# Kernel optimization log

Hardware: AMD Instinct MI355X
Metric: run time of the kernel (lower is better)

## Reference

```python
import jax, jax.numpy as jnp
import numpy as np

B, C, L = 64, 50, 128      # tactic states, context entries per state, AST tokens per entry
V, S = 100008, 128          # vocab (sum of id tables), state/embed dim
OUT = 3


def _gru(h, x, w_ih, w_hh, b_ih, b_hh):
    # torch.nn.GRUCell math
    gi = x @ w_ih.T + b_ih            # [N, 3S]
    gh = h @ w_hh.T + b_hh
    i_r, i_z, i_n = jnp.split(gi, 3, axis=-1)
    h_r, h_z, h_n = jnp.split(gh, 3, axis=-1)
    r = jax.nn.sigmoid(i_r + h_r)
    z = jax.nn.sigmoid(i_z + h_z)
    n = jnp.tanh(i_n + r * h_n)
    return (1.0 - z) * n + z * h


def setup_inputs() -> dict:
    key = jax.random.key(0)
    ks = jax.random.split(key, 16)
    def nrm(k, shape, scale=0.05):
        return jax.random.normal(k, shape, dtype=jnp.float32) * scale
    return {
        "token_ids": jax.random.randint(ks[0], (B, C, L), 0, V),
        "embed_table": nrm(ks[1], (V, S)),
        "ast_w_ih": nrm(ks[2], (3 * S, S)),
        "ast_w_hh": nrm(ks[3], (3 * S, S)),
        "ast_b_ih": nrm(ks[4], (3 * S,)),
        "ast_b_hh": nrm(ks[5], (3 * S,)),
        "ast_init": nrm(ks[6], (1, S)),
        "ctx_w_ih": nrm(ks[7], (3 * S, S)),
        "ctx_w_hh": nrm(ks[8], (3 * S, S)),
        "ctx_b_ih": nrm(ks[9], (3 * S,)),
        "ctx_b_hh": nrm(ks[10], (3 * S,)),
        "ctx_init": nrm(ks[11], (1, S)),
        "proj_w": nrm(ks[12], (S, S + 1)),
        "proj_b": nrm(ks[13], (S,)),
        "final_w": nrm(ks[14], (OUT, S)),
        "final_b": nrm(ks[15], (OUT,)),
    }


def reference(token_ids, embed_table, ast_w_ih, ast_w_hh, ast_b_ih, ast_b_hh,
              ast_init, ctx_w_ih, ctx_w_hh, ctx_b_ih, ctx_b_hh, ctx_init,
              proj_w, proj_b, final_w, final_b):
    Bv, Cv, Lv = token_ids.shape
    Sv = embed_table.shape[-1]
    # --- ast_embed: gather token embeddings, GRU over L steps, batched over B*C ---
    emb = embed_table[token_ids]                                  # [B,C,L,S]
    xs = emb.reshape(Bv * Cv, Lv, Sv).transpose(1, 0, 2)          # [L, B*C, S]
    h0 = jnp.broadcast_to(ast_init, (Bv * Cv, Sv))

    def ast_step(h, x):
        return _gru(h, x, ast_w_ih, ast_w_hh, ast_b_ih, ast_b_hh), None

    hT, _ = jax.lax.scan(ast_step, h0, xs)                        # [B*C, S]
    hT = hT.reshape(Bv, Cv, Sv)

    # --- mask: cat with conclusion indicator (1 for entry 0, else 0), then proj ---
    ind = (jnp.arange(Cv) == 0).astype(hT.dtype)[None, :, None]   # [1,C,1]
    ind = jnp.broadcast_to(ind, (Bv, Cv, 1))
    projs = jnp.concatenate([hT, ind], axis=-1) @ proj_w.T + proj_b  # [B,C,S]

    # --- ctx_embed: GRU over C context entries ---
    cxs = projs.transpose(1, 0, 2)                                # [C,B,S]
    c0 = jnp.broadcast_to(ctx_init, (Bv, Sv))

    def ctx_step(h, x):
        return _gru(h, x, ctx_w_ih, ctx_w_hh, ctx_b_ih, ctx_b_hh), None

    cT, _ = jax.lax.scan(ctx_step, c0, cxs)                       # [B,S]

    # --- final ---
    return cT @ final_w.T + final_b                               # [B,3]
```

## Files before the change

### kernel.cpp

```cpp
#include <hip/hip_runtime.h>


#define V_VOCAB 100008

typedef __attribute__((ext_vector_type(8))) short bf16x8;
typedef __attribute__((ext_vector_type(4))) float f32x4;

__device__ __forceinline__ unsigned pk_bf16(float lo, float hi){
  unsigned r;
  asm("v_cvt_pk_bf16_f32 %0, %1, %2" : "=v"(r) : "v"(lo), "v"(hi));
  return r;
}
__device__ __forceinline__ unsigned short bf1(float x){
  return (unsigned short)pk_bf16(x, x);
}
__device__ __forceinline__ bf16x8 pack8(f32x4 a, f32x4 b){
  union { unsigned u[4]; bf16x8 v; } x;
  x.u[0] = pk_bf16(a[0], a[1]);
  x.u[1] = pk_bf16(a[2], a[3]);
  x.u[2] = pk_bf16(b[0], b[1]);
  x.u[3] = pk_bf16(b[2], b[3]);
  return x.v;
}
__device__ __forceinline__ float bf2f(unsigned bits){
  union { unsigned u; float f; } x; x.u = bits << 16; return x.f;
}
__device__ __forceinline__ float fexp2(float x){ return __builtin_amdgcn_exp2f(x); }
__device__ __forceinline__ float frcp(float x){ return __builtin_amdgcn_rcpf(x); }
__device__ __forceinline__ float sigm(float x){ return frcp(1.f + fexp2(x * -1.44269504089f)); }
__device__ __forceinline__ float tanh_fast(float x){
  float t = fexp2(x * -2.88539008178f);
  return (1.f - t) * frcp(1.f + t);
}
__device__ __forceinline__ int hchunk(int row, int ch){
  return row*128 + ((ch ^ row ^ (row >> 2)) & 15)*8;
}

__global__ __launch_bounds__(256)
void m2_kernel(const float* __restrict__ wcih, const float* __restrict__ pw,
               const float* __restrict__ pb, const float* __restrict__ bcih,
               const float* __restrict__ bchh, float* __restrict__ M2,
               float* __restrict__ b2)
{
  int t = blockIdx.x*256 + threadIdx.x;
  if (t >= 384*130) return;
  int o = t / 130, kk = t % 130;
  const float* wr = wcih + o*128;
  if (kk < 129){
    float acc = 0.f;
    for (int m = 0; m < 128; ++m) acc += wr[m] * pw[m*129 + kk];
    M2[o*132 + kk] = acc;
  } else {
    float acc = bcih[o] + (o < 256 ? bchh[o] : 0.f);
    for (int m = 0; m < 128; ++m) acc += wr[m] * pb[m];
    b2[o] = acc;
  }
}

template<int STEPS, int DEPTH, bool EMB, bool FINAL>
__global__ __launch_bounds__(512, 1)
void gru_kernel(const int* __restrict__ tok_ids,
                const float* __restrict__ emb,
                const float* __restrict__ gi_f32,
                const float* __restrict__ whh,
                const float* __restrict__ wih,
                const float* __restrict__ bih,
                const float* __restrict__ bhh,
                const float* __restrict__ hinit,
                const float* __restrict__ M2,
                const float* __restrict__ b2,
                float* __restrict__ cgi,
                const float* __restrict__ fw,
                const float* __restrict__ fb,
                float* __restrict__ outp)
{
  __shared__ unsigned short hbuf[2][2048];
  __shared__ int toks[EMB ? 2048 : 2];
  __shared__ unsigned short xbuf[EMB ? 4096 : 2];
  const int tid = threadIdx.x;
  const int w = tid >> 6, lane = tid & 63, c = lane & 15, q = lane >> 4;
  const int n0 = blockIdx.x * 16;
  const int w16c = w*16 + c;

  if constexpr (EMB){
    for (int i = tid; i < 2048; i += 512) toks[i] = tok_ids[n0*128 + i] << 9;
  }
  bf16x8 Bh[3][4], Bx[3][4];
#pragma unroll
  for (int g = 0; g < 3; ++g)
#pragma unroll
    for (int kt = 0; kt < 4; ++kt){
      int o = g*128 + w16c;
      const f32x4* ph = (const f32x4*)(whh + o*128 + kt*32 + q*8);
      Bh[g][kt] = pack8(ph[0], ph[1]);
      if constexpr (EMB){
        const f32x4* px = (const f32x4*)(wih + o*128 + kt*32 + q*8);
        Bx[g][kt] = pack8(px[0], px[1]);
      }
    }
  float cr, cz, cin;
  const float bn = bhh[256 + w16c];
  if constexpr (EMB){
    cr  = bih[w16c]       + bhh[w16c];
    cz  = bih[128 + w16c] + bhh[128 + w16c];
    cin = bih[256 + w16c];
  }
  float h_old[4];
  {
    float h0 = hinit[w16c];
#pragma unroll
    for (int r = 0; r < 4; ++r) h_old[r] = h0;
  }
  for (int i = tid; i < 2048; i += 512){
    int row = i >> 7, k = i & 127;
    hbuf[0][hchunk(row, k >> 3) + (k & 7)] = bf1(hinit[k]);
  }
  __syncthreads();

  if constexpr (EMB){
    const int srow = tid >> 5, spos = tid & 31;
    const int sdst = hchunk(srow, spos >> 1) + (spos & 1)*4;
    f32x4 EA, EB, T0, T1;
    auto load_x = [&](f32x4& E, int t){
      int tt = t < STEPS ? t : STEPS - 1;
      E = *(const f32x4*)((const char*)emb
            + (size_t)(unsigned)toks[srow*128 + tt] + spos*16);
    };
    auto write_x = [&](const f32x4& E, int b){
      unsigned long long v = ((unsigned long long)pk_bf16(E[2], E[3]) << 32)
                           | pk_bf16(E[0], E[1]);
      *(unsigned long long*)&xbuf[b*2048 + sdst] = v;
    };
    load_x(T0, 0);
    load_x(T1, 1);
    write_x(T0, 0);
    write_x(T1, 1);
    load_x(EA, 2);
    load_x(EB, 3);
    __syncthreads();
    bf16x8 AxC[4], AxN[4];
#pragma unroll
    for (int kt = 0; kt < 4; ++kt)
      AxC[kt] = *(const bf16x8*)&xbuf[hchunk(c, kt*4 + q)];
    __syncthreads();

    auto body = [&](int s, f32x4& Ew){
      const int cur = s & 1, nxt = cur ^ 1;
      f32x4 D0, D1, D2, D3;
#pragma unroll
      for (int r = 0; r < 4; ++r){ D0[r] = cr; D1[r] = cz; D2[r] = bn; D3[r] = cin; }
#pragma unroll
      for (int kt = 0; kt < 4; ++kt){
        D0 = __builtin_amdgcn_mfma_f32_16x16x32_bf16(AxC[kt], Bx[0][kt], D0, 0,0,0);
        D1 = __builtin_amdgcn_mfma_f32_16x16x32_bf16(AxC[kt], Bx[1][kt], D1, 0,0,0);
        D3 = __builtin_amdgcn_mfma_f32_16x16x32_bf16(AxC[kt], Bx[2][kt], D3, 0,0,0);
      }
      bf16x8 Ah[4];
#pragma unroll
      for (int kt = 0; kt < 4; ++kt)
        Ah[kt] = *(const bf16x8*)&hbuf[cur][hchunk(c, kt*4 + q)];
#pragma unroll
      for (int kt = 0; kt < 4; ++kt){
        D0 = __builtin_amdgcn_mfma_f32_16x16x32_bf16(Ah[kt], Bh[0][kt], D0, 0,0,0);
        D1 = __builtin_amdgcn_mfma_f32_16x16x32_bf16(Ah[kt], Bh[1][kt], D1, 0,0,0);
        D2 = __builtin_amdgcn_mfma_f32_16x16x32_bf16(Ah[kt], Bh[2][kt], D2, 0,0,0);
      }
#pragma unroll
      for (int kt = 0; kt < 4; ++kt)
        AxN[kt] = *(const bf16x8*)&xbuf[nxt*2048 + hchunk(c, kt*4 + q)];
      write_x(Ew, cur);
      load_x(Ew, s + 4);
#pragma unroll
      for (int r = 0; r < 4; ++r){
        float rr = sigm(D0[r]);
        float z  = sigm(D1[r]);
        float nn = tanh_fast(D3[r] + rr * D2[r]);
        h_old[r] = nn + z*(h_old[r] - nn);
      }
#pragma unroll
      for (int r = 0; r < 4; ++r)
        hbuf[nxt][hchunk(q*4 + r, w*2 + (c >> 3)) + (c & 7)] = bf1(h_old[r]);
      asm volatile("s_waitcnt lgkmcnt(0)" ::: "memory");
      __builtin_amdgcn_s_barrier();
#pragma unroll
      for (int kt = 0; kt < 4; ++kt) AxC[kt] = AxN[kt];
    };
#pragma unroll 1
    for (int s = 0; s < STEPS; s += 2){
      body(s,     EA);
      body(s + 1, EB);
    }

    {
      const int fin = STEPS & 1;
      bf16x8 A[4];
#pragma unroll
      for (int kt = 0; kt < 4; ++kt)
        A[kt] = *(const bf16x8*)&hbuf[fin][hchunk(c, kt*4 + q)];
#pragma unroll
      for (int g = 0; g < 3; ++g){
        int o = g*128 + w16c;
        f32x4 D = {0.f,0.f,0.f,0.f};
#pragma unroll
        for (int kt = 0; kt < 4; ++kt){
          const f32x4* p = (const f32x4*)(M2 + o*132 + kt*32 + q*8);
          bf16x8 Bf = pack8(p[0], p[1]);
          D = __builtin_amdgcn_mfma_f32_16x16x32_bf16(A[kt], Bf, D, 0,0,0);
        }
        float bias = b2[o];
        float indv = M2[o*132 + 128];
#pragma unroll
        for (int r = 0; r < 4; ++r){
          int n  = n0 + q*4 + r;
          int cc = n % 50, b = n / 50;
          float vv = D[r] + bias + (cc == 0 ? indv : 0.f);
          cgi[(cc*64 + b)*384 + o] = vv;
        }
      }
    }
  } else {
    unsigned G[DEPTH][12];
    auto load_gi = [&](int d, int S){
#pragma unroll
      for (int r = 0; r < 4; ++r){
        const float* p = gi_f32 + (S*64 + n0 + q*4 + r)*384 + w16c;
        G[d][r]     = __float_as_uint(p[0]);
        G[d][4 + r] = __float_as_uint(p[128]);
        G[d][8 + r] = __float_as_uint(p[256]);
      }
    };
    auto body = [&](int S, int d){
      const int cur = S & 1, nxt = cur ^ 1;
      bf16x8 A[4];
#pragma unroll
      for (int kt = 0; kt < 4; ++kt)
        A[kt] = *(const bf16x8*)&hbuf[cur][hchunk(c, kt*4 + q)];
      f32x4 D[3];
#pragma unroll
      for (int r = 0; r < 4; ++r){
        D[0][r] = __uint_as_float(G[d][r]);
        D[1][r] = __uint_as_float(G[d][4 + r]);
        D[2][r] = bn;
      }
#pragma unroll
      for (int g = 0; g < 3; ++g)
#pragma unroll
        for (int kt = 0; kt < 4; ++kt)
          D[g] = __builtin_amdgcn_mfma_f32_16x16x32_bf16(A[kt], Bh[g][kt], D[g], 0,0,0);
#pragma unroll
      for (int r = 0; r < 4; ++r){
        float gn = __uint_as_float(G[d][8 + r]);
        float rr = sigm(D[0][r]);
        float z  = sigm(D[1][r]);
        float nn = tanh_fast(gn + rr * D[2][r]);
        h_old[r] = nn + z*(h_old[r] - nn);
      }
      if (S + DEPTH < STEPS) load_gi(d, S + DEPTH);
#pragma unroll
      for (int r = 0; r < 4; ++r)
        hbuf[nxt][hchunk(q*4 + r, w*2 + (c >> 3)) + (c & 7)] = bf1(h_old[r]);
      asm volatile("s_waitcnt lgkmcnt(0)" ::: "memory");
      __builtin_amdgcn_s_barrier();
    };
#pragma unroll
    for (int d = 0; d < DEPTH; ++d) load_gi(d, d);
#pragma unroll 1
    for (int s = 0; s < STEPS; s += DEPTH){
#pragma unroll
      for (int d = 0; d < DEPTH; ++d) body(s + d, d);
    }
  }

  if constexpr (FINAL){
    if (tid < 48){
      int row = tid / 3, j = tid % 3;
      float acc = fb[j];
      const int cur = STEPS & 1;
      for (int k = 0; k < 128; ++k)
        acc += bf2f(hbuf[cur][hchunk(row, k >> 3) + (k & 7)]) * fw[j*128 + k];
      outp[(n0 + row)*3 + j] = acc;
    }
  }
}

extern "C" void kernel_launch(void* const* d_in, const int* in_sizes, int n_in,
                              void* d_out, int out_size, void* d_ws, size_t ws_size,
                              hipStream_t stream)
{
  const int*   tok   = (const int*)  d_in[0];
  const float* emb   = (const float*)d_in[1];
  const float* awih  = (const float*)d_in[2];
  const float* awhh  = (const float*)d_in[3];
  const float* abih  = (const float*)d_in[4];
  const float* abhh  = (const float*)d_in[5];
  const float* ainit = (const float*)d_in[6];
  const float* cwih  = (const float*)d_in[7];
  const float* cwhh  = (const float*)d_in[8];
  const float* cbih  = (const float*)d_in[9];
  const float* cbhh  = (const float*)d_in[10];
  const float* cinit = (const float*)d_in[11];
  const float* pw    = (const float*)d_in[12];
  const float* pb    = (const float*)d_in[13];
  const float* fw    = (const float*)d_in[14];
  const float* fb    = (const float*)d_in[15];
  float* out = (float*)d_out;

  char* ws = (char*)d_ws;
  float* cgi = (float*)(ws + 0);
  float* M2  = (float*)(ws + 4915200);
  float* b2  = (float*)(ws + 5117952);

  m2_kernel<<<195, 256, 0, stream>>>(cwih, pw, pb, cbih, cbhh, M2, b2);
  gru_kernel<128, 2, true,  false><<<200, 512, 0, stream>>>(
      tok, emb, nullptr, awhh, awih, abih, abhh, ainit,
      M2, b2, cgi, nullptr, nullptr, nullptr);
  gru_kernel<50,  2, false, true ><<<4,   512, 0, stream>>>(
      nullptr, nullptr, cgi, cwhh, nullptr, nullptr, cbhh, cinit,
      nullptr, nullptr, nullptr, fw, fb, out);
}
```

Measured before the change: 165.4 us.

## Software-pipeline input-gate MFMAs one step ahead of the recurrent GRU path

The AST GRU loop now computes the next step's input projections (x·W_ih for r, z, n) after the current hidden-state update, carrying them in accumulator registers across steps. The serial dependency chain per step shrinks to only the h·W_hh MFMAs plus the gate math, and the independent x MFMAs fill the time between writing h and the barrier. In exchange it holds six extra f32x4 accumulators live across iterations, which raises register pressure. It also adds a static_assert on the ctx loop's unroll depth.

```diff
diff --git a/kernel.cpp b/kernel.cpp
--- a/kernel.cpp
+++ b/kernel.cpp
@@ -138,57 +138,70 @@
     load_x(EA, 2);
     load_x(EB, 3);
     __syncthreads();
-    bf16x8 AxC[4], AxN[4];
-#pragma unroll
-    for (int kt = 0; kt < 4; ++kt)
-      AxC[kt] = *(const bf16x8*)&xbuf[hchunk(c, kt*4 + q)];
+    f32x4 P0, P1, P3, Q0, Q1, Q3;
+    {
+      bf16x8 Ax0[4];
+#pragma unroll
+      for (int kt = 0; kt < 4; ++kt)
+        Ax0[kt] = *(const bf16x8*)&xbuf[hchunk(c, kt*4 + q)];
+#pragma unroll
+      for (int r = 0; r < 4; ++r){ P0[r] = cr; P1[r] = cz; P3[r] = cin; }
+#pragma unroll
+      for (int kt = 0; kt < 4; ++kt){
+        P0 = __builtin_amdgcn_mfma_f32_16x16x32_bf16(Ax0[kt], Bx[0][kt], P0, 0,0,0);
+        P1 = __builtin_amdgcn_mfma_f32_16x16x32_bf16(Ax0[kt], Bx[1][kt], P1, 0,0,0);
+        P3 = __builtin_amdgcn_mfma_f32_16x16x32_bf16(Ax0[kt], Bx[2][kt], P3, 0,0,0);
+      }
+    }
     __syncthreads();
 
-    auto body = [&](int s, f32x4& Ew){
+    auto body = [&](int s, f32x4& C0, f32x4& C1, f32x4& C3,
+                           f32x4& N0, f32x4& N1, f32x4& N3, f32x4& Ew){
       const int cur = s & 1, nxt = cur ^ 1;
-      f32x4 D0, D1, D2, D3;
-#pragma unroll
-      for (int r = 0; r < 4; ++r){ D0[r] = cr; D1[r] = cz; D2[r] = bn; D3[r] = cin; }
+      bf16x8 Ah[4];
+#pragma unroll
+      for (int kt = 0; kt < 4; ++kt)
+        Ah[kt] = *(const bf16x8*)&hbuf[cur][hchunk(c, kt*4 + q)];
+      bf16x8 AxN[4];
+#pragma unroll
+      for (int kt = 0; kt < 4; ++kt)
+        AxN[kt] = *(const bf16x8*)&xbuf[nxt*2048 + hchunk(c, kt*4 + q)];
+      f32x4 D2;
+#pragma unroll
+      for (int r = 0; r < 4; ++r) D2[r] = bn;
 #pragma unroll
       for (int kt = 0; kt < 4; ++kt){
-        D0 = __builtin_amdgcn_mfma_f32_16x16x32_bf16(AxC[kt], Bx[0][kt], D0, 0,0,0);
-        D1 = __builtin_amdgcn_mfma_f32_16x16x32_bf16(AxC[kt], Bx[1][kt], D1, 0,0,0);
-        D3 = __builtin_amdgcn_mfma_f32_16x16x32_bf16(AxC[kt], Bx[2][kt], D3, 0,0,0);
-      }
-      bf16x8 Ah[4];
-#pragma unroll
-      for (int kt = 0; kt < 4; ++kt)
-        Ah[kt] = *(const bf16x8*)&hbuf[cur][hchunk(c, kt*4 + q)];
+        C0 = __builtin_amdgcn_mfma_f32_16x16x32_bf16(Ah[kt], Bh[0][kt], C0, 0,0,0);
+        C1 = __builtin_amdgcn_mfma_f32_16x16x32_bf16(Ah[kt], Bh[1][kt], C1, 0,0,0);
+        D2 = __builtin_amdgcn_mfma_f32_16x16x32_bf16(Ah[kt], Bh[2][kt], D2, 0,0,0);
+      }
+#pragma unroll
+      for (int r = 0; r < 4; ++r){
+        float rr = sigm(C0[r]);
+        float z  = sigm(C1[r]);
+        float nn = tanh_fast(C3[r] + rr * D2[r]);
+        h_old[r] = nn + z*(h_old[r] - nn);
+      }
+#pragma unroll
+      for (int r = 0; r < 4; ++r)
+        hbuf[nxt][hchunk(q*4 + r, w*2 + (c >> 3)) + (c & 7)] = bf1(h_old[r]);
+#pragma unroll
+      for (int r = 0; r < 4; ++r){ N0[r] = cr; N1[r] = cz; N3[r] = cin; }
 #pragma unroll
       for (int kt = 0; kt < 4; ++kt){
-        D0 = __builtin_amdgcn_mfma_f32_16x16x32_bf16(Ah[kt], Bh[0][kt], D0, 0,0,0);
-        D1 = __builtin_amdgcn_mfma_f32_16x16x32_bf16(Ah[kt], Bh[1][kt], D1, 0,0,0);
-        D2 = __builtin_amdgcn_mfma_f32_16x16x32_bf16(Ah[kt], Bh[2][kt], D2, 0,0,0);
-      }
-#pragma unroll
-      for (int kt = 0; kt < 4; ++kt)
-        AxN[kt] = *(const bf16x8*)&xbuf[nxt*2048 + hchunk(c, kt*4 + q)];
+        N0 = __builtin_amdgcn_mfma_f32_16x16x32_bf16(AxN[kt], Bx[0][kt], N0, 0,0,0);
+        N1 = __builtin_amdgcn_mfma_f32_16x16x32_bf16(AxN[kt], Bx[1][kt], N1, 0,0,0);
+        N3 = __builtin_amdgcn_mfma_f32_16x16x32_bf16(AxN[kt], Bx[2][kt], N3, 0,0,0);
+      }
       write_x(Ew, cur);
       load_x(Ew, s + 4);
-#pragma unroll
-      for (int r = 0; r < 4; ++r){
-        float rr = sigm(D0[r]);
-        float z  = sigm(D1[r]);
-        float nn = tanh_fast(D3[r] + rr * D2[r]);
-        h_old[r] = nn + z*(h_old[r] - nn);
-      }
-#pragma unroll
-      for (int r = 0; r < 4; ++r)
-        hbuf[nxt][hchunk(q*4 + r, w*2 + (c >> 3)) + (c & 7)] = bf1(h_old[r]);
       asm volatile("s_waitcnt lgkmcnt(0)" ::: "memory");
       __builtin_amdgcn_s_barrier();
-#pragma unroll
-      for (int kt = 0; kt < 4; ++kt) AxC[kt] = AxN[kt];
     };
 #pragma unroll 1
     for (int s = 0; s < STEPS; s += 2){
-      body(s,     EA);
-      body(s + 1, EB);
+      body(s,     P0, P1, P3, Q0, Q1, Q3, EA);
+      body(s + 1, Q0, Q1, Q3, P0, P1, P3, EB);
     }
 
     {
@@ -219,6 +232,7 @@
       }
     }
   } else {
+    static_assert(EMB || (STEPS % DEPTH == 0), "ctx loop unrolls by DEPTH");
     unsigned G[DEPTH][12];
     auto load_gi = [&](int d, int S){
 #pragma unroll
```

Result: no change. 168.1 us (+1.6%).
